# Kernel optimization log

Measured on AMD Instinct MI355X. Metric: run time of the kernel, lower is better.

The kernel has to match this reference:

```python
import jax, jax.numpy as jnp
import numpy as np
import math

EMB_DIM = 3        # positional embedding dim of the implicit Hyena filter
FILTER_ORDER = 64  # hidden width of the implicit filter MLP


def rmsnorm(x, w, eps=1e-8):
    return x * jax.lax.rsqrt(jnp.mean(x * x, axis=-1, keepdims=True) + eps) * w


def _implicit_filter(L, D, mlp_w1, mlp_b1, freq1, mlp_w2, mlp_b2, freq2, mlp_w3):
    # positional embedding (emb_dim=3): [t, Re exp(-i f w), Im exp(-i f w)], bands=1
    t = jnp.linspace(0.0, 1.0, L)[:, None]                               # (L,1)
    w = 2.0 * math.pi * jnp.linspace(0.0, L - 1.0, L)[:, None] / L       # (L,1)
    f = jnp.linspace(1e-4, 0.0, 1)[None, :]                              # (1,1)
    ang = f * w
    z = jnp.concatenate([t, jnp.cos(ang), -jnp.sin(ang)], axis=-1)       # (L,3)
    # implicit filter MLP with Sin activations
    h = jnp.sin(freq1 * (z @ mlp_w1.T + mlp_b1))
    h = jnp.sin(freq2 * (h @ mlp_w2.T + mlp_b2))
    h = h @ mlp_w3.T                                                     # (L,D)
    # exponential modulation (modulate=True)
    fast, slow, target = 0.3, 1.5, 1e-2
    max_decay = math.log(target) / fast
    min_decay = math.log(target) / slow
    deltas = jnp.linspace(min_decay, max_decay, D)[None, :]              # (1,D)
    h = h * jnp.exp(-t * jnp.abs(deltas))
    return h.T                                                           # (D,L)


def _fftconv(v, k, bias):
    # causal long conv via zero-padded FFT. v: (B,D,L), k: (D,L), bias: (D,)
    L = v.shape[-1]
    n = 2 * L
    kf = jnp.fft.rfft(k, n=n) / n
    y = jnp.fft.irfft(jnp.fft.rfft(v, n=n) * kf, n=n, norm="forward")[..., :L]
    return y + v * bias[None, :, None]


def _block(x, norm_in_w, in_proj_w, in_proj_b, short_filter_w, short_filter_b,
           mlp_w1, mlp_b1, freq1, mlp_w2, mlp_b2, freq2, mlp_w3, filter_bias,
           out_proj_w, out_proj_b, norm_w, ffn_w1, ffn_b1, ffn_w2, ffn_b2):
    B, L, D = x.shape
    xn = rmsnorm(x, norm_in_w)
    # Hyena operator
    u = (xn @ in_proj_w.T + in_proj_b).transpose(0, 2, 1)                # (B,3D,L)
    uc = jax.lax.conv_general_dilated(
        u, short_filter_w, (1,), [(2, 0)],
        feature_group_count=3 * D, dimension_numbers=("NCH", "OIH", "NCH"))
    uc = uc + short_filter_b[None, :, None]                              # causal k=3 depthwise
    x0, x1, v = jnp.split(uc, 3, axis=1)                                 # (B,D,L) each
    k = _implicit_filter(L, D, mlp_w1, mlp_b1, freq1, mlp_w2, mlp_b2, freq2, mlp_w3)
    v = _fftconv(v * x1, k, filter_bias)                                 # gate, long conv
    y = (v * x0).transpose(0, 2, 1) @ out_proj_w.T + out_proj_b          # gate, out proj
    # residual + FFN
    h = y + x
    o = rmsnorm(h, norm_w)
    o = jax.nn.gelu(o @ ffn_w1.T + ffn_b1) @ ffn_w2.T + ffn_b2
    return o + h


def setup_inputs():
    key = jax.random.key(0)
    B, L, D = 4, 2048, 1024
    ks = jax.random.split(key, 12)

    def lin(k, out_d, in_d):
        return jax.random.normal(k, (out_d, in_d), jnp.float32) * (1.0 / math.sqrt(in_d))

    return {
        "x": jax.random.normal(ks[0], (B, L, D), jnp.float32),
        "norm_in_w": jnp.ones((D,), jnp.float32),
        "in_proj_w": lin(ks[1], 3 * D, D),
        "in_proj_b": jnp.zeros((3 * D,), jnp.float32),
        "short_filter_w": jax.random.normal(ks[2], (3 * D, 1, 3), jnp.float32) / math.sqrt(3.0),
        "short_filter_b": jnp.zeros((3 * D,), jnp.float32),
        "mlp_w1": lin(ks[3], FILTER_ORDER, EMB_DIM),
        "mlp_b1": jnp.zeros((FILTER_ORDER,), jnp.float32),
        "freq1": jnp.ones((FILTER_ORDER,), jnp.float32),
        "mlp_w2": lin(ks[4], FILTER_ORDER, FILTER_ORDER),
        "mlp_b2": jnp.zeros((FILTER_ORDER,), jnp.float32),
        "freq2": jnp.ones((FILTER_ORDER,), jnp.float32),
        "mlp_w3": lin(ks[5], D, FILTER_ORDER),
        "filter_bias": jax.random.normal(ks[6], (D,), jnp.float32),
        "out_proj_w": lin(ks[7], D, D),
        "out_proj_b": jnp.zeros((D,), jnp.float32),
        "norm_w": jnp.ones((D,), jnp.float32),
        "ffn_w1": lin(ks[8], 2 * D, D),
        "ffn_b1": jnp.zeros((2 * D,), jnp.float32),
        "ffn_w2": lin(ks[9], D, 2 * D),
        "ffn_b2": jnp.zeros((D,), jnp.float32),
    }


def reference(x, norm_in_w, in_proj_w, in_proj_b, short_filter_w, short_filter_b,
              mlp_w1, mlp_b1, freq1, mlp_w2, mlp_b2, freq2, mlp_w3, filter_bias,
              out_proj_w, out_proj_b, norm_w, ffn_w1, ffn_b1, ffn_w2, ffn_b2):
    return _block(x, norm_in_w, in_proj_w, in_proj_b, short_filter_w, short_filter_b,
                  mlp_w1, mlp_b1, freq1, mlp_w2, mlp_b2, freq2, mlp_w3, filter_bias,
                  out_proj_w, out_proj_b, norm_w, ffn_w1, ffn_b1, ffn_w2, ffn_b2)
```

## Files before the change

kernel.cpp:

```cpp
#include <hip/hip_runtime.h>
#include <hip/hip_bf16.h>
#include <cstddef>

#define BB 4
#define LL 2048
#define DD 1024
#define MM (BB*LL)
#define KF_STRIDE 2056

#define SWZ(a) ((a) ^ (((a) >> 4) & 12))

typedef __bf16 bf16_t;
typedef __attribute__((ext_vector_type(8))) __bf16 bf16x8;
typedef __attribute__((ext_vector_type(4))) __bf16 bf16x4;
typedef __attribute__((ext_vector_type(4))) float f32x4;

#define GLD_LDS16(gp, lp) __builtin_amdgcn_global_load_lds(                 \
    (const __attribute__((address_space(1))) unsigned int*)(gp),            \
    (__attribute__((address_space(3))) unsigned int*)(lp), 16, 0, 0)

__device__ __forceinline__ float gelu_tanh(float x) {
    const float c = 0.7978845608028654f;
    float t = tanhf(c * (x + 0.044715f * x * x * x));
    return 0.5f * x * (1.0f + t);
}

__device__ __forceinline__ float2 cmul(float2 a, float2 b) {
    return make_float2(a.x * b.x - a.y * b.y, a.x * b.y + a.y * b.x);
}
__device__ __forceinline__ float2 cadd(float2 a, float2 b) {
    return make_float2(a.x + b.x, a.y + b.y);
}
__device__ __forceinline__ float2 csub(float2 a, float2 b) {
    return make_float2(a.x - b.x, a.y - b.y);
}
__device__ __forceinline__ float2 cmuli(float2 z, float s) {
    return make_float2(-s * z.y, s * z.x);
}

__global__ __launch_bounds__(256) void cast_all_kernel(
    const float* __restrict__ s0, const float* __restrict__ s1,
    const float* __restrict__ s2, const float* __restrict__ s3,
    bf16_t* __restrict__ d0, bf16_t* __restrict__ d1,
    bf16_t* __restrict__ d2, bf16_t* __restrict__ d3)
{
    const int b = blockIdx.x;
    const float* s; bf16_t* d; int base;
    if (b < 3072)      { s = s0; d = d0; base = b; }
    else if (b < 4096) { s = s1; d = d1; base = b - 3072; }
    else if (b < 6144) { s = s2; d = d2; base = b - 4096; }
    else               { s = s3; d = d3; base = b - 6144; }
    const int i = (base * 256 + threadIdx.x) * 4;
    const float4 v = *(const float4*)(s + i);
    bf16x4 o;
    o[0] = (bf16_t)v.x; o[1] = (bf16_t)v.y; o[2] = (bf16_t)v.z; o[3] = (bf16_t)v.w;
    *(bf16x4*)(d + i) = o;
}

__global__ __launch_bounds__(256) void rmsnorm_bf16_kernel(
    const float* __restrict__ in, const float* __restrict__ w,
    bf16_t* __restrict__ out)
{
    const int row = blockIdx.x;
    const float4* ip = (const float4*)(in + (size_t)row * DD);
    float4 v = ip[threadIdx.x];
    float ss = v.x*v.x + v.y*v.y + v.z*v.z + v.w*v.w;
    #pragma unroll
    for (int off = 32; off > 0; off >>= 1) ss += __shfl_down(ss, off, 64);
    __shared__ float sums[4];
    const int wid = threadIdx.x >> 6;
    if ((threadIdx.x & 63) == 0) sums[wid] = ss;
    __syncthreads();
    const float tot = sums[0] + sums[1] + sums[2] + sums[3];
    const float scale = rsqrtf(tot * (1.0f / (float)DD) + 1e-8f);
    const float4 wv = ((const float4*)w)[threadIdx.x];
    bf16x4 o;
    o[0] = (bf16_t)(v.x * scale * wv.x);
    o[1] = (bf16_t)(v.y * scale * wv.y);
    o[2] = (bf16_t)(v.z * scale * wv.z);
    o[3] = (bf16_t)(v.w * scale * wv.w);
    *(bf16x4*)(out + (size_t)row * DD + threadIdx.x * 4) = o;
}

template<int EPI, bool BF16OUT, bool BIASROW = false>
__global__ __launch_bounds__(256) void gemm_mfma_kernel(
    const bf16_t* __restrict__ A,
    const bf16_t* __restrict__ W,
    const float* __restrict__ bias,
    const float* __restrict__ res,
    float* __restrict__ Cf,
    bf16_t* __restrict__ Cb,
    int M, int N, int K)
{
    __shared__ __align__(16) bf16_t As[2][128 * 64];
    __shared__ __align__(16) bf16_t Ws[2][128 * 64];
    const int tid  = threadIdx.x;
    const int bm   = blockIdx.y * 128;
    const int bn   = blockIdx.x * 128;
    const int lane = tid & 63;
    const int wave = tid >> 6;
    const int wr   = (wave >> 1) * 64;
    const int wc   = (wave & 1) * 64;

    int srow[4], sqg[4];
    #pragma unroll
    for (int c = 0; c < 4; ++c) {
        const int p = c * 256 + tid;
        srow[c] = p >> 3;
        sqg[c]  = (((p & 7) ^ (srow[c] & 7)) << 3);
    }

    f32x4 acc[4][4] = {};

    const int fr = lane & 15;
    const int fc = (lane >> 4) * 8;

    const int nt = K >> 6;

    #pragma unroll
    for (int c = 0; c < 4; ++c) {
        GLD_LDS16(A + (size_t)(bm + srow[c]) * K + sqg[c],
                  &As[0][c * 2048 + tid * 8]);
        GLD_LDS16(W + (size_t)(bn + srow[c]) * K + sqg[c],
                  &Ws[0][c * 2048 + tid * 8]);
    }
    __syncthreads();

    int cur = 0;
    for (int t = 0; t < nt; ++t) {
        if (t + 1 < nt) {
            const int k0 = (t + 1) << 6;
            #pragma unroll
            for (int c = 0; c < 4; ++c) {
                GLD_LDS16(A + (size_t)(bm + srow[c]) * K + k0 + sqg[c],
                          &As[cur ^ 1][c * 2048 + tid * 8]);
                GLD_LDS16(W + (size_t)(bn + srow[c]) * K + k0 + sqg[c],
                          &Ws[cur ^ 1][c * 2048 + tid * 8]);
            }
        }
        #pragma unroll
        for (int ks = 0; ks < 64; ks += 32) {
            const int q = (ks + fc) >> 3;
            bf16x8 af[4], wf[4];
            #pragma unroll
            for (int i = 0; i < 4; ++i) {
                const int r = wr + i*16 + fr;
                af[i] = *(const bf16x8*)(&As[cur][r * 64 + ((q ^ (r & 7)) << 3)]);
            }
            #pragma unroll
            for (int j = 0; j < 4; ++j) {
                const int r = wc + j*16 + fr;
                wf[j] = *(const bf16x8*)(&Ws[cur][r * 64 + ((q ^ (r & 7)) << 3)]);
            }
            __builtin_amdgcn_s_setprio(1);
            #pragma unroll
            for (int i = 0; i < 4; ++i)
                #pragma unroll
                for (int j = 0; j < 4; ++j)
                    acc[i][j] = __builtin_amdgcn_mfma_f32_16x16x32_bf16(
                        af[i], wf[j], acc[i][j], 0, 0, 0);
            __builtin_amdgcn_s_setprio(0);
        }
        __syncthreads();
        cur ^= 1;
    }

    const int fq = lane >> 4;
    #pragma unroll
    for (int i = 0; i < 4; ++i) {
        const int row0 = bm + wr + i*16 + fq*4;
        #pragma unroll
        for (int j = 0; j < 4; ++j) {
            const int col = bn + wc + j*16 + fr;
            const float bcol = BIASROW ? 0.0f : bias[col];
            #pragma unroll
            for (int r = 0; r < 4; ++r) {
                float v = acc[i][j][r] + (BIASROW ? bias[row0 + r] : bcol);
                if constexpr (EPI == 2) v = gelu_tanh(v);
                if constexpr (EPI == 1) v += res[(size_t)(row0 + r) * N + col];
                if constexpr (BF16OUT)
                    Cb[(size_t)(row0 + r) * N + col] = (bf16_t)v;
                else
                    Cf[(size_t)(row0 + r) * N + col] = v;
            }
        }
    }
}

__global__ __launch_bounds__(256) void shortfilter_kernel(
    const bf16_t* __restrict__ ut, const float* __restrict__ sw,
    const float* __restrict__ sb, bf16_t* __restrict__ x0t,
    float* __restrict__ vin)
{
    const int d = blockIdx.x;
    const int c0 = d, c1 = DD + d, c2 = 2 * DD + d;
    const float w0a = sw[c0*3+0], w0b = sw[c0*3+1], w0c = sw[c0*3+2], b0 = sb[c0];
    const float w1a = sw[c1*3+0], w1b = sw[c1*3+1], w1c = sw[c1*3+2], b1 = sb[c1];
    const float w2a = sw[c2*3+0], w2b = sw[c2*3+1], w2c = sw[c2*3+2], b2 = sb[c2];
    const bf16_t* r0 = ut + (size_t)c0 * MM;
    const bf16_t* r1 = ut + (size_t)c1 * MM;
    const bf16_t* r2 = ut + (size_t)c2 * MM;
    bf16_t* o0 = x0t + (size_t)d * MM;
    float*  o1 = vin + (size_t)d * MM;
    for (int m0 = threadIdx.x * 8; m0 < MM; m0 += 2048) {
        const int l0 = m0 & (LL - 1);
        const bf16x8 a0 = *(const bf16x8*)(r0 + m0);
        const bf16x8 a1 = *(const bf16x8*)(r1 + m0);
        const bf16x8 a2 = *(const bf16x8*)(r2 + m0);
        float u0[10], u1[10], u2[10];
        u0[0] = u0[1] = u1[0] = u1[1] = u2[0] = u2[1] = 0.0f;
        if (l0 != 0) {
            u0[0] = (float)r0[m0-2]; u0[1] = (float)r0[m0-1];
            u1[0] = (float)r1[m0-2]; u1[1] = (float)r1[m0-1];
            u2[0] = (float)r2[m0-2]; u2[1] = (float)r2[m0-1];
        }
        #pragma unroll
        for (int i = 0; i < 8; ++i) {
            u0[i+2] = (float)a0[i];
            u1[i+2] = (float)a1[i];
            u2[i+2] = (float)a2[i];
        }
        bf16x8 ov;
        float v1o[8];
        #pragma unroll
        for (int i = 0; i < 8; ++i) {
            const float v0 = w0c*u0[i+2] + w0b*u0[i+1] + w0a*u0[i] + b0;
            const float v1 = w1c*u1[i+2] + w1b*u1[i+1] + w1a*u1[i] + b1;
            const float v2 = w2c*u2[i+2] + w2b*u2[i+1] + w2a*u2[i] + b2;
            ov[i] = (bf16_t)v0;
            v1o[i] = v2 * v1;
        }
        *(bf16x8*)(o0 + m0) = ov;
        *(float4*)(o1 + m0)     = make_float4(v1o[0], v1o[1], v1o[2], v1o[3]);
        *(float4*)(o1 + m0 + 4) = make_float4(v1o[4], v1o[5], v1o[6], v1o[7]);
    }
}

__global__ __launch_bounds__(256) void filtermlp_kernel(
    const float* __restrict__ w1, const float* __restrict__ b1,
    const float* __restrict__ f1, const float* __restrict__ w2,
    const float* __restrict__ b2, const float* __restrict__ f2,
    float* __restrict__ h2t)
{
    __shared__ float w2s[64 * 64];
    __shared__ float h1s[64][32];
    const int tid = threadIdx.x;
    #pragma unroll
    for (int i = 0; i < 4; ++i)
        ((float4*)w2s)[tid + 256 * i] = ((const float4*)w2)[tid + 256 * i];

    const int l0 = blockIdx.x * 32;
    const int l  = tid & 31;
    const float fl = (float)(l0 + l);
    const float t   = fl * (1.0f / (float)(LL - 1));
    const float ang = 1e-4f * 6.283185307179586f * fl * (1.0f / (float)LL);
    const float z0 = t, z1 = cosf(ang), z2 = -sinf(ang);

    #pragma unroll
    for (int i = 0; i < 8; ++i) {
        const int j = (tid >> 5) + 8 * i;
        const float s = w1[j*3+0]*z0 + w1[j*3+1]*z1 + w1[j*3+2]*z2 + b1[j];
        h1s[j][l] = sinf(f1[j] * s);
    }
    __syncthreads();

    const int jb = (tid >> 5) * 8;
    float acc[8];
    #pragma unroll
    for (int i = 0; i < 8; ++i) acc[i] = b2[jb + i];
    #pragma unroll
    for (int jj = 0; jj < 64; jj += 4) {
        const float h0 = h1s[jj + 0][l];
        const float h1v = h1s[jj + 1][l];
        const float h2v = h1s[jj + 2][l];
        const float h3 = h1s[jj + 3][l];
        #pragma unroll
        for (int i = 0; i < 8; ++i) {
            const float4 wv = *(const float4*)&w2s[(jb + i) * 64 + jj];
            acc[i] += wv.x * h0 + wv.y * h1v + wv.z * h2v + wv.w * h3;
        }
    }
    #pragma unroll
    for (int i = 0; i < 8; ++i)
        h2t[(size_t)(jb + i) * LL + l0 + l] = sinf(f2[jb + i] * acc[i]);
}

__global__ __launch_bounds__(256) void filtermod_kernel(
    const float* __restrict__ w3, const float* __restrict__ h2t,
    float* __restrict__ kfilt)
{
    __shared__ float w3s[32 * 64];
    const int d0 = blockIdx.y * 32;
    const int l  = blockIdx.x * 256 + threadIdx.x;
    for (int i = threadIdx.x; i < 32 * 64; i += 256) w3s[i] = w3[d0 * 64 + i];
    __syncthreads();
    float acc[32] = {};
    for (int j = 0; j < 64; ++j) {
        const float v = h2t[j * LL + l];
        #pragma unroll
        for (int dd = 0; dd < 32; ++dd) acc[dd] += w3s[dd*64 + j] * v;
    }
    const float t = (float)l / (float)(LL - 1);
    const float min_decay = -3.0701134573253944f;
    const float max_decay = -15.350567286626972f;
    #pragma unroll
    for (int dd = 0; dd < 32; ++dd) {
        const int d = d0 + dd;
        const float delta = fabsf(min_decay + (max_decay - min_decay) * (float)d / (float)(DD - 1));
        kfilt[(size_t)d * LL + l] = acc[dd] * expf(-t * delta);
    }
}

template<int SIGN>
__device__ __forceinline__ void fft4096_r8_ip(float2* __restrict__ buf)
{
    const float fs = (float)SIGN;
    const float RH = 0.7071067811865476f;
    const int tid = threadIdx.x;
    #pragma unroll
    for (int t = 0; t < 4; ++t) {
        const int ls = 3 * t;
        const int s  = 1 << ls;
        const float theta = fs * 6.283185307179586f / (float)(4096 >> ls);
        float2 a[8];
        #pragma unroll
        for (int m = 0; m < 8; ++m) a[m] = buf[SWZ(tid + m * 512)];
        __syncthreads();
        const int p = tid >> ls;
        const int q = tid & (s - 1);
        float sn, cs;
        __sincosf(theta * (float)p, &sn, &cs);
        const float2 W1 = make_float2(cs, sn);
        const float2 W2 = cmul(W1, W1);
        const float2 W3 = cmul(W2, W1);
        const float2 W4 = cmul(W2, W2);
        const float2 W5 = cmul(W4, W1);
        const float2 W6 = cmul(W4, W2);
        const float2 W7 = cmul(W4, W3);
        const float2 es = cadd(a[0], a[4]), ed = csub(a[0], a[4]);
        const float2 fs2 = cadd(a[2], a[6]), fd = csub(a[2], a[6]);
        const float2 E0 = cadd(es, fs2);
        const float2 E1 = cadd(ed, cmuli(fd, fs));
        const float2 E2 = csub(es, fs2);
        const float2 E3 = csub(ed, cmuli(fd, fs));
        const float2 os = cadd(a[1], a[5]), od = csub(a[1], a[5]);
        const float2 gs = cadd(a[3], a[7]), gd = csub(a[3], a[7]);
        const float2 O0 = cadd(os, gs);
        const float2 O1 = cadd(od, cmuli(gd, fs));
        const float2 O2 = csub(os, gs);
        const float2 O3 = csub(od, cmuli(gd, fs));
        const float2 T0 = O0;
        const float2 T1 = make_float2(RH * (O1.x - fs * O1.y), RH * (fs * O1.x + O1.y));
        const float2 T2 = cmuli(O2, fs);
        const float2 T3 = make_float2(RH * (-O3.x - fs * O3.y), RH * (fs * O3.x - O3.y));
        const int o = q + (p << (ls + 3));
        buf[SWZ(o)]         = cadd(E0, T0);
        buf[SWZ(o + s)]     = cmul(W1, cadd(E1, T1));
        buf[SWZ(o + 2*s)]   = cmul(W2, cadd(E2, T2));
        buf[SWZ(o + 3*s)]   = cmul(W3, cadd(E3, T3));
        buf[SWZ(o + 4*s)]   = cmul(W4, csub(E0, T0));
        buf[SWZ(o + 5*s)]   = cmul(W5, csub(E1, T1));
        buf[SWZ(o + 6*s)]   = cmul(W6, csub(E2, T2));
        buf[SWZ(o + 7*s)]   = cmul(W7, csub(E3, T3));
        __syncthreads();
    }
}

__global__ __launch_bounds__(512, 4) void kfft_kernel(
    const float* __restrict__ kfilt, float2* __restrict__ Kf)
{
    __shared__ float2 fb[4096];
    const int d0 = blockIdx.x * 2;
    const float* k0 = kfilt + (size_t)d0 * LL;
    const float* k1 = k0 + LL;
    const float inv = 1.0f / 4096.0f;
    const int tid = threadIdx.x;
    for (int i = tid; i < 2048; i += 512) {
        fb[SWZ(i)]        = make_float2(k0[i] * inv, k1[i] * inv);
        fb[SWZ(i + 2048)] = make_float2(0.f, 0.f);
    }
    __syncthreads();
    fft4096_r8_ip<-1>(fb);
    float2* o0 = Kf + (size_t)d0 * KF_STRIDE;
    float2* o1 = o0 + KF_STRIDE;
    for (int k = tid; k <= 2048; k += 512) {
        const float2 z1 = fb[SWZ(k)];
        const float2 z2 = fb[SWZ((4096 - k) & 4095)];
        o0[k] = make_float2(0.5f * (z1.x + z2.x), 0.5f * (z1.y - z2.y));
        o1[k] = make_float2(0.5f * (z1.y + z2.y), 0.5f * (z2.x - z1.x));
    }
}

__global__ __launch_bounds__(512, 4) void fftconv_kernel(
    float* __restrict__ vio, const float2* __restrict__ Kf,
    const float* __restrict__ fbias)
{
    __shared__ float2 fb[4096];
    const int blk = blockIdx.x;
    const int d   = blk >> 1;
    float* v1 = vio + (size_t)(2 * blk) * LL;
    float* v2 = v1 + LL;
    const int tid = threadIdx.x;
    for (int i = tid; i < 2048; i += 512) {
        fb[SWZ(i)]        = make_float2(v1[i], v2[i]);
        fb[SWZ(i + 2048)] = make_float2(0.f, 0.f);
    }
    __syncthreads();
    fft4096_r8_ip<-1>(fb);
    const float2* kf = Kf + (size_t)d * KF_STRIDE;
    for (int i = tid; i < 4096; i += 512) {
        float2 k;
        if (i <= 2048) k = kf[i];
        else { const float2 t = kf[4096 - i]; k = make_float2(t.x, -t.y); }
        fb[SWZ(i)] = cmul(fb[SWZ(i)], k);
    }
    __syncthreads();
    fft4096_r8_ip<1>(fb);
    const float bias = fbias[d];
    for (int i = tid; i < 2048; i += 512) {
        const float2 zy = fb[SWZ(i)];
        v1[i] = zy.x + bias * v1[i];
        v2[i] = zy.y + bias * v2[i];
    }
}

__global__ __launch_bounds__(256) void gate_transpose_kernel(
    const float* __restrict__ y, const bf16_t* __restrict__ x0t,
    bf16_t* __restrict__ g)
{
    __shared__ float tile[32][33];
    const int b  = blockIdx.z;
    const int l0 = blockIdx.x * 32;
    const int d0 = blockIdx.y * 32;
    const int tx  = threadIdx.x & 31;
    const int tyb = threadIdx.x >> 5;
    #pragma unroll
    for (int i = 0; i < 4; ++i) {
        const int dy = tyb + i * 8;
        const size_t src = ((size_t)(d0 + dy) * BB + b) * LL + l0 + tx;
        tile[dy][tx] = y[src] * (float)x0t[src];
    }
    __syncthreads();
    #pragma unroll
    for (int i = 0; i < 4; ++i) {
        const int ly = tyb + i * 8;
        g[((size_t)(b * LL + l0 + ly)) * DD + d0 + tx] = (bf16_t)tile[tx][ly];
    }
}

extern "C" void kernel_launch(void* const* d_in, const int* in_sizes, int n_in,
                              void* d_out, int out_size, void* d_ws, size_t ws_size,
                              hipStream_t stream)
{
    (void)in_sizes; (void)n_in; (void)out_size; (void)ws_size;
    const float* x   = (const float*)d_in[0];
    const float* nw0 = (const float*)d_in[1];
    const float* ipw = (const float*)d_in[2];
    const float* ipb = (const float*)d_in[3];
    const float* sfw = (const float*)d_in[4];
    const float* sfb = (const float*)d_in[5];
    const float* w1  = (const float*)d_in[6];
    const float* b1  = (const float*)d_in[7];
    const float* f1  = (const float*)d_in[8];
    const float* w2  = (const float*)d_in[9];
    const float* b2  = (const float*)d_in[10];
    const float* f2  = (const float*)d_in[11];
    const float* w3  = (const float*)d_in[12];
    const float* fbv = (const float*)d_in[13];
    const float* opw = (const float*)d_in[14];
    const float* opb = (const float*)d_in[15];
    const float* nw1 = (const float*)d_in[16];
    const float* fw1 = (const float*)d_in[17];
    const float* fb1 = (const float*)d_in[18];
    const float* fw2 = (const float*)d_in[19];
    const float* fb2 = (const float*)d_in[20];
    float* out = (float*)d_out;

    float* ws = (float*)d_ws;
    bf16_t* utb    = (bf16_t*)ws;
    bf16_t* gatedb = (bf16_t*)ws;
    float*  h      = ws + 4194304;
    bf16_t* midb   = (bf16_t*)(ws + 12582912);
    bf16_t* xnb    = (bf16_t*)(ws + 25165824);
    bf16_t* x0tb   = (bf16_t*)(ws + 29360128);
    float*  vio    = ws + 37748736;
    float*  kfilt  = ws + 46137344;
    float2* Kf     = (float2*)(ws + 48234496);
    bf16_t* ipwb   = (bf16_t*)(ws + 52445184);
    bf16_t* opwb   = ipwb + 3145728;
    bf16_t* fw1b   = opwb + 1048576;
    bf16_t* fw2b   = fw1b + 2097152;
    float*  h2t    = ws + 56639488;

    cast_all_kernel<<<8192, 256, 0, stream>>>(ipw, opw, fw1, fw2,
                                              ipwb, opwb, fw1b, fw2b);
    filtermlp_kernel<<<LL/32, 256, 0, stream>>>(w1, b1, f1, w2, b2, f2, h2t);
    filtermod_kernel<<<dim3(LL/256, DD/32), 256, 0, stream>>>(w3, h2t, kfilt);
    kfft_kernel<<<DD/2, 512, 0, stream>>>(kfilt, Kf);
    rmsnorm_bf16_kernel<<<MM, 256, 0, stream>>>(x, nw0, xnb);
    gemm_mfma_kernel<0, true, true><<<dim3(MM/128, 3072/128), 256, 0, stream>>>(
        ipwb, xnb, ipb, nullptr, nullptr, utb, 3*DD, MM, DD);
    shortfilter_kernel<<<DD, 256, 0, stream>>>(utb, sfw, sfb, x0tb, vio);
    fftconv_kernel<<<BB*DD/2, 512, 0, stream>>>(vio, Kf, fbv);
    gate_transpose_kernel<<<dim3(LL/32, DD/32, BB), 256, 0, stream>>>(vio, x0tb, gatedb);
    gemm_mfma_kernel<1, false><<<dim3(DD/128, MM/128), 256, 0, stream>>>(
        gatedb, opwb, opb, x, h, nullptr, MM, DD, DD);
    rmsnorm_bf16_kernel<<<MM, 256, 0, stream>>>(h, nw1, xnb);
    gemm_mfma_kernel<2, true><<<dim3(2*DD/128, MM/128), 256, 0, stream>>>(
        xnb, fw1b, fb1, nullptr, nullptr, midb, MM, 2*DD, DD);
    gemm_mfma_kernel<1, false><<<dim3(DD/128, MM/128), 256, 0, stream>>>(
        midb, fw2b, fb2, h, out, nullptr, MM, DD, 2*DD);
}
```

Measured before the change: 481.5 us.

## Add 256x256-tile 8-wave GEMM kernel for in-proj and FFN-up GEMMs

Adds a new bf16 MFMA GEMM kernel using 256x256 output tiles with 512 threads, double-buffered LDS staged by direct global-to-LDS loads with an XOR swizzle. Each K-step is split into four quadrant sub-phases so loads for the next tile interleave with MFMA work, using explicit barriers, vmcnt waits and setprio. It replaces the 128x128 GEMM for the in-projection and the first FFN GEMM to raise arithmetic intensity and overlap memory traffic with compute. The larger tiles use 128 KB of LDS per block and produce fewer blocks, which may lower occupancy or cause wave-quantization effects.

```diff
diff --git a/kernel.cpp b/kernel.cpp
--- a/kernel.cpp
+++ b/kernel.cpp
@@ -18,6 +18,10 @@
 #define GLD_LDS16(gp, lp) __builtin_amdgcn_global_load_lds(                 \
     (const __attribute__((address_space(1))) unsigned int*)(gp),            \
     (__attribute__((address_space(3))) unsigned int*)(lp), 16, 0, 0)
+
+#define BARX() do { __builtin_amdgcn_s_barrier();                           \
+                    __builtin_amdgcn_sched_barrier(0); } while (0)
+#define VMW(N) asm volatile("s_waitcnt vmcnt(" #N ")" ::: "memory")
 
 __device__ __forceinline__ float gelu_tanh(float x) {
     const float c = 0.7978845608028654f;
@@ -185,6 +189,159 @@
             }
         }
     }
+}
+
+__device__ __forceinline__ void stage_half256(
+    const bf16_t* __restrict__ G, int grow0, int K, int k0,
+    bf16_t* __restrict__ L, int hf, int tid)
+{
+    #pragma unroll
+    for (int cc = 0; cc < 2; ++cc) {
+        const int p   = (hf * 2 + cc) * 512 + tid;
+        const int row = p >> 3;
+        const int qg  = (((p & 7) ^ (row & 7)) << 3);
+        GLD_LDS16(G + (size_t)(grow0 + row) * K + k0 + qg, L + p * 8);
+    }
+}
+
+#define LOAD_A256(QR)                                                        \
+    _Pragma("unroll")                                                        \
+    for (int ks = 0; ks < 2; ++ks)                                           \
+      _Pragma("unroll")                                                      \
+      for (int mi = 0; mi < 4; ++mi) {                                       \
+        const int r = (QR)*128 + vm*64 + mi*16 + fr;                         \
+        a[ks][mi] = *(const bf16x8*)(Ac + r*64 + ((((ks*4)+kq) ^ (r&7))<<3)); \
+      }
+
+#define LOAD_B256(QC, BV)                                                    \
+    _Pragma("unroll")                                                        \
+    for (int ks = 0; ks < 2; ++ks)                                           \
+      _Pragma("unroll")                                                      \
+      for (int nj = 0; nj < 2; ++nj) {                                       \
+        const int r = (QC)*128 + vn*32 + nj*16 + fr;                         \
+        BV[ks][nj] = *(const bf16x8*)(Wc + r*64 + ((((ks*4)+kq) ^ (r&7))<<3)); \
+      }
+
+#define MFMA16(ACC, BV)                                                      \
+    __builtin_amdgcn_s_setprio(1);                                           \
+    _Pragma("unroll")                                                        \
+    for (int ks = 0; ks < 2; ++ks)                                           \
+      _Pragma("unroll")                                                      \
+      for (int mi = 0; mi < 4; ++mi)                                         \
+        _Pragma("unroll")                                                    \
+        for (int nj = 0; nj < 2; ++nj)                                       \
+          ACC[mi][nj] = __builtin_amdgcn_mfma_f32_16x16x32_bf16(             \
+              a[ks][mi], BV[ks][nj], ACC[mi][nj], 0, 0, 0);                  \
+    __builtin_amdgcn_s_setprio(0);
+
+template<int EPI, bool BF16OUT, bool BIASROW = false>
+__global__ __launch_bounds__(512, 2) void gemm256_kernel(
+    const bf16_t* __restrict__ A,
+    const bf16_t* __restrict__ W,
+    const float* __restrict__ bias,
+    float* __restrict__ Cf,
+    bf16_t* __restrict__ Cb,
+    int M, int N, int K)
+{
+    __shared__ __align__(16) bf16_t As[2][256 * 64];
+    __shared__ __align__(16) bf16_t Ws[2][256 * 64];
+    const int tid  = threadIdx.x;
+    const int bm   = blockIdx.y * 256;
+    const int bn   = blockIdx.x * 256;
+    const int lane = tid & 63;
+    const int wave = tid >> 6;
+    const int vm   = wave >> 2;
+    const int vn   = wave & 3;
+    const int fr   = lane & 15;
+    const int kq   = lane >> 4;
+
+    bf16x8 a[2][4], b0[2][2], b1[2][2];
+    f32x4 acc00[4][2] = {}, acc01[4][2] = {}, acc10[4][2] = {}, acc11[4][2] = {};
+
+    const int nt = K >> 6;
+
+    stage_half256(A, bm, K, 0, &As[0][0], 0, tid);
+    stage_half256(W, bn, K, 0, &Ws[0][0], 0, tid);
+    stage_half256(W, bn, K, 0, &Ws[0][0], 1, tid);
+    stage_half256(A, bm, K, 0, &As[0][0], 1, tid);
+    VMW(4);
+    BARX();
+
+    for (int t = 0; t < nt - 1; ++t) {
+        const int c = t & 1, o = c ^ 1;
+        const bf16_t* Ac = &As[c][0];
+        const bf16_t* Wc = &Ws[c][0];
+        const int kn = (t + 1) << 6;
+        LOAD_A256(0); LOAD_B256(0, b0);
+        stage_half256(A, bm, K, kn, &As[o][0], 0, tid);
+        VMW(4);
+        BARX();
+        MFMA16(acc00, b0);
+        BARX();
+        LOAD_B256(1, b1);
+        stage_half256(W, bn, K, kn, &Ws[o][0], 0, tid);
+        VMW(4);
+        BARX();
+        MFMA16(acc01, b1);
+        BARX();
+        LOAD_A256(1);
+        stage_half256(W, bn, K, kn, &Ws[o][0], 1, tid);
+        BARX();
+        MFMA16(acc11, b1);
+        BARX();
+        stage_half256(A, bm, K, kn, &As[o][0], 1, tid);
+        VMW(4);
+        BARX();
+        MFMA16(acc10, b0);
+        BARX();
+    }
+    {
+        const int c = (nt - 1) & 1;
+        const bf16_t* Ac = &As[c][0];
+        const bf16_t* Wc = &Ws[c][0];
+        LOAD_A256(0); LOAD_B256(0, b0);
+        VMW(2);
+        BARX();
+        MFMA16(acc00, b0);
+        BARX();
+        LOAD_B256(1, b1);
+        VMW(0);
+        BARX();
+        MFMA16(acc01, b1);
+        BARX();
+        LOAD_A256(1);
+        BARX();
+        MFMA16(acc11, b1);
+        BARX();
+        MFMA16(acc10, b0);
+        BARX();
+    }
+
+    const int fq = lane >> 4;
+    #define EPILOG256(ACC, QR, QC)                                           \
+        _Pragma("unroll")                                                    \
+        for (int mi = 0; mi < 4; ++mi) {                                     \
+          const int row0 = bm + (QR)*128 + vm*64 + mi*16 + fq*4;             \
+          _Pragma("unroll")                                                  \
+          for (int nj = 0; nj < 2; ++nj) {                                   \
+            const int col = bn + (QC)*128 + vn*32 + nj*16 + fr;              \
+            const float bcol = BIASROW ? 0.0f : bias[col];                   \
+            _Pragma("unroll")                                                \
+            for (int r = 0; r < 4; ++r) {                                    \
+              float v = ACC[mi][nj][r] + (BIASROW ? bias[row0 + r] : bcol);  \
+              if constexpr (EPI == 2) v = gelu_tanh(v);                      \
+              if constexpr (BF16OUT)                                         \
+                  Cb[(size_t)(row0 + r) * N + col] = (bf16_t)v;              \
+              else                                                           \
+                  Cf[(size_t)(row0 + r) * N + col] = v;                      \
+            }                                                                \
+          }                                                                  \
+        }
+    EPILOG256(acc00, 0, 0);
+    EPILOG256(acc01, 0, 1);
+    EPILOG256(acc11, 1, 1);
+    EPILOG256(acc10, 1, 0);
+    #undef EPILOG256
 }
 
 __global__ __launch_bounds__(256) void shortfilter_kernel(
@@ -498,16 +655,16 @@
     filtermod_kernel<<<dim3(LL/256, DD/32), 256, 0, stream>>>(w3, h2t, kfilt);
     kfft_kernel<<<DD/2, 512, 0, stream>>>(kfilt, Kf);
     rmsnorm_bf16_kernel<<<MM, 256, 0, stream>>>(x, nw0, xnb);
-    gemm_mfma_kernel<0, true, true><<<dim3(MM/128, 3072/128), 256, 0, stream>>>(
-        ipwb, xnb, ipb, nullptr, nullptr, utb, 3*DD, MM, DD);
+    gemm256_kernel<0, true, true><<<dim3(MM/256, 3072/256), 512, 0, stream>>>(
+        ipwb, xnb, ipb, nullptr, utb, 3*DD, MM, DD);
     shortfilter_kernel<<<DD, 256, 0, stream>>>(utb, sfw, sfb, x0tb, vio);
     fftconv_kernel<<<BB*DD/2, 512, 0, stream>>>(vio, Kf, fbv);
     gate_transpose_kernel<<<dim3(LL/32, DD/32, BB), 256, 0, stream>>>(vio, x0tb, gatedb);
     gemm_mfma_kernel<1, false><<<dim3(DD/128, MM/128), 256, 0, stream>>>(
         gatedb, opwb, opb, x, h, nullptr, MM, DD, DD);
     rmsnorm_bf16_kernel<<<MM, 256, 0, stream>>>(h, nw1, xnb);
-    gemm_mfma_kernel<2, true><<<dim3(2*DD/128, MM/128), 256, 0, stream>>>(
-        xnb, fw1b, fb1, nullptr, nullptr, midb, MM, 2*DD, DD);
+    gemm256_kernel<2, true><<<dim3(2*DD/256, MM/256), 512, 0, stream>>>(
+        xnb, fw1b, fb1, nullptr, midb, MM, 2*DD, DD);
     gemm_mfma_kernel<1, false><<<dim3(DD/128, MM/128), 256, 0, stream>>>(
         midb, fw2b, fb2, h, out, nullptr, MM, DD, 2*DD);
 }
```

Measured after the change: 494.8 us. 2.8% more time.
